# Kernel tuning notes

Hardware: AMD Instinct MI355X
Metric: run time of the kernel (lower is better)

The kernel has to match this reference:

```python
import jax, jax.numpy as jnp
import numpy as np


def gcn_conv(x, src, dst, norm, W, b, n_nodes):
    # PyG GCNConv: out[dst] = sum_edges norm * (x @ W)[src] + b
    h = x @ W                      # [N, F_out]
    msg = h[src] * norm[:, None]   # [E', F_out] gather + scale
    out = jax.ops.segment_sum(msg, dst, num_segments=n_nodes)
    return out + b


def _gcn_norm(edge_index, n_nodes):
    # add self loops, compute symmetric normalization deg^-1/2[src]*deg^-1/2[dst]
    loop = jnp.arange(n_nodes, dtype=edge_index.dtype)
    src = jnp.concatenate([edge_index[0], loop])
    dst = jnp.concatenate([edge_index[1], loop])
    deg = jnp.zeros((n_nodes,), jnp.float32).at[dst].add(1.0)
    dinv = jnp.where(deg > 0, jax.lax.rsqrt(deg), 0.0)
    norm = dinv[src] * dinv[dst]
    return src, dst, norm


def setup_inputs() -> dict:
    key = jax.random.key(0)
    ks = jax.random.split(key, 5)
    N, E, C_in, C_out = 50000, 800000, 128, 32
    H = 2 * C_out
    x = jax.random.normal(ks[0], (N, C_in), jnp.float32)
    edge_index = jax.random.randint(ks[1], (2, E), 0, N, jnp.int64)
    s1 = 1.0 / np.sqrt(C_in)
    s2 = 1.0 / np.sqrt(H)
    W1 = jax.random.uniform(ks[2], (C_in, H), jnp.float32, -s1, s1)
    b1 = jnp.zeros((H,), jnp.float32)
    W_mu = jax.random.uniform(ks[3], (H, C_out), jnp.float32, -s2, s2)
    b_mu = jnp.zeros((C_out,), jnp.float32)
    W_ls = jax.random.uniform(ks[4], (H, C_out), jnp.float32, -s2, s2)
    b_ls = jnp.zeros((C_out,), jnp.float32)
    return {"x": x, "edge_index": edge_index, "W1": W1, "b1": b1,
            "W_mu": W_mu, "b_mu": b_mu, "W_ls": W_ls, "b_ls": b_ls}


def reference(x, edge_index, W1, b1, W_mu, b_mu, W_ls, b_ls):
    n_nodes = x.shape[0]
    src, dst, norm = _gcn_norm(edge_index, n_nodes)
    h = jax.nn.relu(gcn_conv(x, src, dst, norm, W1, b1, n_nodes))
    mu = gcn_conv(h, src, dst, norm, W_mu, b_mu, n_nodes)
    logstd = gcn_conv(h, src, dst, norm, W_ls, b_ls, n_nodes)
    return mu, logstd
```

## Files before the change

kernel.cpp:

```cpp
#include <hip/hip_runtime.h>
#include <hip/hip_fp16.h>
#include <math.h>


typedef unsigned int uint;
typedef unsigned short ushort;
typedef __attribute__((ext_vector_type(8))) short short8;
typedef __attribute__((ext_vector_type(4))) float f32x4;

__device__ __forceinline__ ushort f2bf(float x) {
    uint u = __float_as_uint(x);
    u += 0x7fffu + ((u >> 16) & 1u);
    return (ushort)(u >> 16);
}
__device__ __forceinline__ float bf2f(ushort h) {
    return __uint_as_float((uint)h << 16);
}

__global__ __launch_bounds__(256) void k_hist(
        const int* __restrict__ dst, int* __restrict__ bcount, int E) {
    __shared__ int h[256];
    const int tid = threadIdx.x;
    h[tid] = 0;
    __syncthreads();
    const int base = blockIdx.x * 2048;
    #pragma unroll
    for (int k = 0; k < 8; ++k) {
        int i = base + k * 256 + tid;
        if (i < E) {
            int d = __builtin_nontemporal_load(dst + i);
            atomicAdd(&h[d >> 8], 1);
        }
    }
    __syncthreads();
    if (h[tid]) atomicAdd(&bcount[tid], h[tid]);
}

__global__ __launch_bounds__(256) void k_scatterA(
        const int* __restrict__ src, const int* __restrict__ dst,
        const int* __restrict__ bcount, int* __restrict__ bcursor,
        uint* __restrict__ recs, int E) {
    __shared__ int h[256];
    __shared__ int p[256];
    __shared__ int rb[256];
    const int tid = threadIdx.x;
    h[tid] = 0;
    __syncthreads();
    const int base = blockIdx.x * 2048;
    uint rec[8]; int rk[8];
    #pragma unroll
    for (int k = 0; k < 8; ++k) {
        int i = base + k * 256 + tid;
        if (i < E) {
            int s = __builtin_nontemporal_load(src + i);
            int d = __builtin_nontemporal_load(dst + i);
            int b = d >> 8;
            rec[k] = (uint)s | ((uint)(d & 255) << 16) | ((uint)b << 24);
            rk[k] = atomicAdd(&h[b], 1);
        }
    }
    int v = bcount[tid];
    p[tid] = v;
    __syncthreads();
    #pragma unroll
    for (int off = 1; off < 256; off <<= 1) {
        int x = (tid >= off) ? p[tid - off] : 0;
        __syncthreads();
        p[tid] += x;
        __syncthreads();
    }
    const int excl = p[tid] - v;
    const int hv = h[tid];
    rb[tid] = excl + (hv ? atomicAdd(&bcursor[tid], hv) : 0);
    __syncthreads();
    #pragma unroll
    for (int k = 0; k < 8; ++k) {
        int i = base + k * 256 + tid;
        if (i < E) recs[rb[rec[k] >> 24] + rk[k]] = rec[k];
    }
}

__global__ __launch_bounds__(256, 4) void k_phaseB(
        const uint* __restrict__ recs, const int* __restrict__ bcount,
        int* __restrict__ row_ptr, float* __restrict__ dinv,
        ushort* __restrict__ edges, int N, int E, int NBUCK) {
    __shared__ int h[256];
    __shared__ int p[256];
    __shared__ uint rstage[8192];
    const int tid = threadIdx.x;
    const int bx  = blockIdx.x;
    int v = bcount[tid];
    p[tid] = v;
    h[tid] = 0;
    __syncthreads();
    #pragma unroll
    for (int off = 1; off < 256; off <<= 1) {
        int x = (tid >= off) ? p[tid - off] : 0;
        __syncthreads();
        p[tid] += x;
        __syncthreads();
    }
    const int cnt = bcount[bx];
    const int bs  = p[bx] - cnt;
    const bool stg = (cnt <= 8192);
    for (int i = tid; i < cnt; i += 256) {
        uint r = recs[bs + i];
        if (stg) rstage[i] = r;
        atomicAdd(&h[(r >> 16) & 255], 1);
    }
    __syncthreads();
    v = h[tid];
    p[tid] = v;
    __syncthreads();
    #pragma unroll
    for (int off = 1; off < 256; off <<= 1) {
        int x = (tid >= off) ? p[tid - off] : 0;
        __syncthreads();
        p[tid] += x;
        __syncthreads();
    }
    const int excl = p[tid] - v;
    const int node = bx * 256 + tid;
    if (node < N) {
        row_ptr[node] = bs + excl;
        dinv[node] = rsqrtf((float)(v + 1));
    }
    if (bx == NBUCK - 1 && tid == 0) row_ptr[N] = E;
    h[tid] = excl;
    __syncthreads();
    for (int i = tid; i < cnt; i += 256) {
        uint r = stg ? rstage[i] : recs[bs + i];
        int pos = atomicAdd(&h[(r >> 16) & 255], 1);
        edges[bs + pos] = (ushort)(r & 0xffffu);
    }
}

__global__ __launch_bounds__(256, 4) void k_gemm(
        const float* __restrict__ x, const float* __restrict__ W1,
        const float* __restrict__ dinv, ushort* __restrict__ hp, int N) {
    __shared__ ushort Wt[64][136];
    const int tid = threadIdx.x;
    #pragma unroll
    for (int it = 0; it < 8; ++it) {
        int idx = (it * 256 + tid) * 4;
        int k = idx >> 6, c = idx & 63;
        float4 wv = *(const float4*)(W1 + idx);
        Wt[c + 0][k] = f2bf(wv.x);
        Wt[c + 1][k] = f2bf(wv.y);
        Wt[c + 2][k] = f2bf(wv.z);
        Wt[c + 3][k] = f2bf(wv.w);
    }
    __syncthreads();
    const int w = tid >> 6, l = tid & 63;
    const int m = l & 15, q = l >> 4;
    const int row0 = blockIdx.x * 64 + w * 16;
    const size_t arow = (size_t)min(row0 + m, N - 1);
    f32x4 acc0 = {0.f, 0.f, 0.f, 0.f}, acc1 = acc0, acc2 = acc0, acc3 = acc0;
    #pragma unroll
    for (int kc = 0; kc < 4; ++kc) {
        const int kofs = kc * 32 + q * 8;
        const float4* xr = (const float4*)(x + arow * 128 + kofs);
        float4 xa = xr[0], xb = xr[1];
        short8 a;
        a[0] = (short)f2bf(xa.x); a[1] = (short)f2bf(xa.y);
        a[2] = (short)f2bf(xa.z); a[3] = (short)f2bf(xa.w);
        a[4] = (short)f2bf(xb.x); a[5] = (short)f2bf(xb.y);
        a[6] = (short)f2bf(xb.z); a[7] = (short)f2bf(xb.w);
        short8 b0 = *(const short8*)&Wt[m][kofs];
        short8 b1 = *(const short8*)&Wt[m + 16][kofs];
        short8 b2 = *(const short8*)&Wt[m + 32][kofs];
        short8 b3 = *(const short8*)&Wt[m + 48][kofs];
        acc0 = __builtin_amdgcn_mfma_f32_16x16x32_bf16(a, b0, acc0, 0, 0, 0);
        acc1 = __builtin_amdgcn_mfma_f32_16x16x32_bf16(a, b1, acc1, 0, 0, 0);
        acc2 = __builtin_amdgcn_mfma_f32_16x16x32_bf16(a, b2, acc2, 0, 0, 0);
        acc3 = __builtin_amdgcn_mfma_f32_16x16x32_bf16(a, b3, acc3, 0, 0, 0);
    }
    #pragma unroll
    for (int r = 0; r < 4; ++r) {
        int row = row0 + q * 4 + r;
        if (row >= N) continue;
        float dv = dinv[row];
        ushort* hr = hp + (size_t)row * 64 + m;
        hr[0]  = f2bf(acc0[r] * dv);
        hr[16] = f2bf(acc1[r] * dv);
        hr[32] = f2bf(acc2[r] * dv);
        hr[48] = f2bf(acc3[r] * dv);
    }
}

__device__ __forceinline__ void gather_grp8(
        const uint* __restrict__ hp, const ushort* __restrict__ edges,
        int beg, int end, int E, int sl, float4& a0, float4& a1) {
    for (int base = beg; base < end; base += 8) {
        const int mrec = (int)edges[min(base + sl, E - 1)];
        const int cnt = end - base;
        if (cnt >= 8) {
            #pragma unroll
            for (int i = 0; i < 8; ++i) {
                const int r = __shfl(mrec, i, 8);
                const uint4 v = *(const uint4*)(hp + (size_t)r * 32 + 4 * sl);
                a0.x += __uint_as_float(v.x << 16);
                a0.y += __uint_as_float(v.x & 0xffff0000u);
                a0.z += __uint_as_float(v.y << 16);
                a0.w += __uint_as_float(v.y & 0xffff0000u);
                a1.x += __uint_as_float(v.z << 16);
                a1.y += __uint_as_float(v.z & 0xffff0000u);
                a1.z += __uint_as_float(v.w << 16);
                a1.w += __uint_as_float(v.w & 0xffff0000u);
            }
        } else {
            #pragma unroll
            for (int i = 0; i < 7; ++i) {
                const int r = __shfl(mrec, min(i, cnt - 1), 8);
                uint4 v = *(const uint4*)(hp + (size_t)r * 32 + 4 * sl);
                if (i >= cnt) { v.x = 0u; v.y = 0u; v.z = 0u; v.w = 0u; }
                a0.x += __uint_as_float(v.x << 16);
                a0.y += __uint_as_float(v.x & 0xffff0000u);
                a0.z += __uint_as_float(v.y << 16);
                a0.w += __uint_as_float(v.y & 0xffff0000u);
                a1.x += __uint_as_float(v.z << 16);
                a1.y += __uint_as_float(v.z & 0xffff0000u);
                a1.z += __uint_as_float(v.w << 16);
                a1.w += __uint_as_float(v.w & 0xffff0000u);
            }
        }
    }
}

__global__ __launch_bounds__(256, 6) void k_gather1(
        const uint* __restrict__ hp, const int* __restrict__ row_ptr,
        const ushort* __restrict__ edges, const float* __restrict__ dinv,
        const float* __restrict__ b1, uint* __restrict__ ho, int N, int E) {
    const int lane = threadIdx.x & 63;
    const int sl = lane & 7;
    const int n = blockIdx.x * 32 + ((threadIdx.x >> 6) << 3) + (lane >> 3);
    const int nc = min(n, N - 1);
    const int beg = row_ptr[nc], end = row_ptr[nc + 1];
    float4 a0 = {0.f, 0.f, 0.f, 0.f}, a1 = a0;
    gather_grp8(hp, edges, beg, end, E, sl, a0, a1);
    const float dv = dinv[nc];
    const uint4 sv = *(const uint4*)(hp + (size_t)nc * 32 + 4 * sl);
    const float4 bA = ((const float4*)b1)[2 * sl];
    const float4 bB = ((const float4*)b1)[2 * sl + 1];
    float s0 = a0.x + bf2f((ushort)sv.x);
    float s1 = a0.y + bf2f((ushort)(sv.x >> 16));
    float s2 = a0.z + bf2f((ushort)sv.y);
    float s3 = a0.w + bf2f((ushort)(sv.y >> 16));
    float s4 = a1.x + bf2f((ushort)sv.z);
    float s5 = a1.y + bf2f((ushort)(sv.z >> 16));
    float s6 = a1.z + bf2f((ushort)sv.w);
    float s7 = a1.w + bf2f((ushort)(sv.w >> 16));
    float h0 = fmaxf(fmaf(dv, s0, bA.x), 0.f) * dv;
    float h1 = fmaxf(fmaf(dv, s1, bA.y), 0.f) * dv;
    float h2 = fmaxf(fmaf(dv, s2, bA.z), 0.f) * dv;
    float h3 = fmaxf(fmaf(dv, s3, bA.w), 0.f) * dv;
    float h4 = fmaxf(fmaf(dv, s4, bB.x), 0.f) * dv;
    float h5 = fmaxf(fmaf(dv, s5, bB.y), 0.f) * dv;
    float h6 = fmaxf(fmaf(dv, s6, bB.z), 0.f) * dv;
    float h7 = fmaxf(fmaf(dv, s7, bB.w), 0.f) * dv;
    if (n < N) {
        uint4 o;
        o.x = (uint)f2bf(h0) | ((uint)f2bf(h1) << 16);
        o.y = (uint)f2bf(h2) | ((uint)f2bf(h3) << 16);
        o.z = (uint)f2bf(h4) | ((uint)f2bf(h5) << 16);
        o.w = (uint)f2bf(h6) | ((uint)f2bf(h7) << 16);
        *(uint4*)(ho + (size_t)n * 32 + 4 * sl) = o;
    }
}

__global__ __launch_bounds__(256, 6) void k_gather2(
        const uint* __restrict__ hp, const int* __restrict__ row_ptr,
        const ushort* __restrict__ edges, const float* __restrict__ dinv,
        const float* __restrict__ Wmu, const float* __restrict__ Wls,
        const float* __restrict__ bmu, const float* __restrict__ bls,
        float* __restrict__ out, int N, int E) {
    __shared__ __align__(16) float hs[4][8][64];
    const int lane = threadIdx.x & 63;
    const int sl = lane & 7, grp = lane >> 3;
    const int w = threadIdx.x >> 6;
    const int n = blockIdx.x * 32 + (w << 3) + grp;
    const int nc = min(n, N - 1);
    const int beg = row_ptr[nc], end = row_ptr[nc + 1];
    float4 a0 = {0.f, 0.f, 0.f, 0.f}, a1 = a0;
    gather_grp8(hp, edges, beg, end, E, sl, a0, a1);
    const float dv = dinv[nc];
    const uint4 sv = *(const uint4*)(hp + (size_t)nc * 32 + 4 * sl);
    float4 gA, gB;
    gA.x = dv * (a0.x + bf2f((ushort)sv.x));
    gA.y = dv * (a0.y + bf2f((ushort)(sv.x >> 16)));
    gA.z = dv * (a0.z + bf2f((ushort)sv.y));
    gA.w = dv * (a0.w + bf2f((ushort)(sv.y >> 16)));
    gB.x = dv * (a1.x + bf2f((ushort)sv.z));
    gB.y = dv * (a1.y + bf2f((ushort)(sv.z >> 16)));
    gB.z = dv * (a1.z + bf2f((ushort)sv.w));
    gB.w = dv * (a1.w + bf2f((ushort)(sv.w >> 16)));
    *(float4*)&hs[w][grp][8 * sl]     = gA;
    *(float4*)&hs[w][grp][8 * sl + 4] = gB;
    const float* Wsel = (lane < 32) ? (Wmu + lane) : (Wls + (lane - 32));
    const float bias  = (lane < 32) ? bmu[lane] : bls[lane - 32];
    #pragma unroll
    for (int p = 0; p < 2; ++p) {
        float c0 = 0.f, c1 = 0.f, c2 = 0.f, c3 = 0.f;
        #pragma unroll 4
        for (int k = 0; k < 64; ++k) {
            float wv = Wsel[k * 32];
            c0 = fmaf(hs[w][p * 4 + 0][k], wv, c0);
            c1 = fmaf(hs[w][p * 4 + 1][k], wv, c1);
            c2 = fmaf(hs[w][p * 4 + 2][k], wv, c2);
            c3 = fmaf(hs[w][p * 4 + 3][k], wv, c3);
        }
        const int n0 = blockIdx.x * 32 + (w << 3) + p * 4;
        float cs[4] = {c0, c1, c2, c3};
        #pragma unroll
        for (int gg = 0; gg < 4; ++gg) {
            int nn = n0 + gg;
            if (nn >= N) break;
            float t = cs[gg] + bias;
            if (lane < 32) out[(size_t)nn * 32 + lane] = t;
            else           out[(size_t)N * 32 + (size_t)nn * 32 + (lane - 32)] = t;
        }
    }
}

extern "C" void kernel_launch(void* const* d_in, const int* in_sizes, int n_in,
                              void* d_out, int out_size, void* d_ws, size_t ws_size,
                              hipStream_t stream) {
    const float* x   = (const float*)d_in[0];
    const int*   ei  = (const int*)d_in[1];
    const float* W1  = (const float*)d_in[2];
    const float* b1  = (const float*)d_in[3];
    const float* Wmu = (const float*)d_in[4];
    const float* bmu = (const float*)d_in[5];
    const float* Wls = (const float*)d_in[6];
    const float* bls = (const float*)d_in[7];
    float* out = (float*)d_out;

    const int N = in_sizes[0] / 128;
    const int E = in_sizes[1] / 2;
    const int* src = ei;
    const int* dst = ei + E;
    const int HB    = (E + 2047) / 2048;
    const int NBUCK = (N + 255) / 256;
    const int GB    = (N + 63) / 64;
    const int NG    = (N + 31) / 32;

    char* w = (char*)d_ws;
    auto carve = [&](size_t bytes) { char* p = w; w += (bytes + 1023) & ~(size_t)1023; return p; };
    int*    bcount  = (int*)   carve(512 * 4);
    int*    bcursor = bcount + 256;
    uint*   recs    = (uint*)  carve((size_t)E * 4);
    int*    row_ptr = (int*)   carve((size_t)(N + 1) * 4);
    float*  dinv    = (float*) carve((size_t)N * 4);
    ushort* edges   = (ushort*)carve((size_t)E * 2);
    ushort* h_pre   = (ushort*)carve((size_t)N * 64 * 2);
    ushort* h_mid   = (ushort*)carve((size_t)N * 64 * 2);

    hipMemsetAsync(bcount, 0, 512 * 4, stream);
    k_hist    <<<HB, 256, 0, stream>>>(dst, bcount, E);
    k_scatterA<<<HB, 256, 0, stream>>>(src, dst, bcount, bcursor, recs, E);
    k_phaseB  <<<NBUCK, 256, 0, stream>>>(recs, bcount, row_ptr, dinv, edges, N, E, NBUCK);
    k_gemm    <<<GB, 256, 0, stream>>>(x, W1, dinv, h_pre, N);
    k_gather1 <<<NG, 256, 0, stream>>>((const uint*)h_pre, row_ptr, edges, dinv,
                                       b1, (uint*)h_mid, N, E);
    k_gather2 <<<NG, 256, 0, stream>>>((const uint*)h_mid, row_ptr, edges, dinv,
                                       Wmu, Wls, bmu, bls, out, N, E);
}
```

Measured before the change: 182.1 us.

## Split hidden features into two 32-wide halves and gather each half separately

The GEMM now writes the 64-wide bf16 hidden features as two separate 32-column arrays. Each SpMM gather pass runs once per half, with 4 lanes per node instead of 8. This shrinks the per-pass working set (N×64B per half), so gathered rows are more likely to stay in L2/MALL cache. The second layer stores the first half's aggregation as fp32 and combines it with the second half in a final kernel that uses an XOR-swizzled shared buffer to avoid LDS bank conflicts. In exchange, the edge list and row pointers are read twice per layer, there are extra launches, and an fp32 intermediate is written and read back.

Measured after the change: 201.7 us. 10.7% more time.

```diff
diff --git a/kernel.cpp b/kernel.cpp
--- a/kernel.cpp
+++ b/kernel.cpp
@@ -137,7 +137,8 @@
 
 __global__ __launch_bounds__(256, 4) void k_gemm(
         const float* __restrict__ x, const float* __restrict__ W1,
-        const float* __restrict__ dinv, ushort* __restrict__ hp, int N) {
+        const float* __restrict__ dinv, ushort* __restrict__ hpA,
+        ushort* __restrict__ hpB, int N) {
     __shared__ ushort Wt[64][136];
     const int tid = threadIdx.x;
     #pragma unroll
@@ -180,68 +181,68 @@
         int row = row0 + q * 4 + r;
         if (row >= N) continue;
         float dv = dinv[row];
-        ushort* hr = hp + (size_t)row * 64 + m;
-        hr[0]  = f2bf(acc0[r] * dv);
-        hr[16] = f2bf(acc1[r] * dv);
-        hr[32] = f2bf(acc2[r] * dv);
-        hr[48] = f2bf(acc3[r] * dv);
-    }
-}
-
-__device__ __forceinline__ void gather_grp8(
-        const uint* __restrict__ hp, const ushort* __restrict__ edges,
-        int beg, int end, int E, int sl, float4& a0, float4& a1) {
+        ushort* hrA = hpA + (size_t)row * 32 + m;
+        hrA[0]  = f2bf(acc0[r] * dv);
+        hrA[16] = f2bf(acc1[r] * dv);
+        ushort* hrB = hpB + (size_t)row * 32 + m;
+        hrB[0]  = f2bf(acc2[r] * dv);
+        hrB[16] = f2bf(acc3[r] * dv);
+    }
+}
+
+__device__ __forceinline__ void acc8(const uint4 v, float4& a0, float4& a1) {
+    a0.x += __uint_as_float(v.x << 16);
+    a0.y += __uint_as_float(v.x & 0xffff0000u);
+    a0.z += __uint_as_float(v.y << 16);
+    a0.w += __uint_as_float(v.y & 0xffff0000u);
+    a1.x += __uint_as_float(v.z << 16);
+    a1.y += __uint_as_float(v.z & 0xffff0000u);
+    a1.z += __uint_as_float(v.w << 16);
+    a1.w += __uint_as_float(v.w & 0xffff0000u);
+}
+
+__device__ __forceinline__ void gather_grp4(
+        const uint* __restrict__ rows, const ushort* __restrict__ edges,
+        int beg, int end, int E, int j, float4& a0, float4& a1) {
     for (int base = beg; base < end; base += 8) {
-        const int mrec = (int)edges[min(base + sl, E - 1)];
         const int cnt = end - base;
+        const int m0 = (int)edges[min(base + j, E - 1)];
+        const int m1 = (int)edges[min(base + 4 + j, E - 1)];
         if (cnt >= 8) {
             #pragma unroll
             for (int i = 0; i < 8; ++i) {
-                const int r = __shfl(mrec, i, 8);
-                const uint4 v = *(const uint4*)(hp + (size_t)r * 32 + 4 * sl);
-                a0.x += __uint_as_float(v.x << 16);
-                a0.y += __uint_as_float(v.x & 0xffff0000u);
-                a0.z += __uint_as_float(v.y << 16);
-                a0.w += __uint_as_float(v.y & 0xffff0000u);
-                a1.x += __uint_as_float(v.z << 16);
-                a1.y += __uint_as_float(v.z & 0xffff0000u);
-                a1.z += __uint_as_float(v.w << 16);
-                a1.w += __uint_as_float(v.w & 0xffff0000u);
+                const int r = __shfl(i < 4 ? m0 : m1, i & 3, 4);
+                const uint4 v = *(const uint4*)(rows + (size_t)r * 16 + 4 * j);
+                acc8(v, a0, a1);
             }
         } else {
             #pragma unroll
             for (int i = 0; i < 7; ++i) {
-                const int r = __shfl(mrec, min(i, cnt - 1), 8);
-                uint4 v = *(const uint4*)(hp + (size_t)r * 32 + 4 * sl);
+                const int e = min(i, cnt - 1);
+                const int r = __shfl(e < 4 ? m0 : m1, e & 3, 4);
+                uint4 v = *(const uint4*)(rows + (size_t)r * 16 + 4 * j);
                 if (i >= cnt) { v.x = 0u; v.y = 0u; v.z = 0u; v.w = 0u; }
-                a0.x += __uint_as_float(v.x << 16);
-                a0.y += __uint_as_float(v.x & 0xffff0000u);
-                a0.z += __uint_as_float(v.y << 16);
-                a0.w += __uint_as_float(v.y & 0xffff0000u);
-                a1.x += __uint_as_float(v.z << 16);
-                a1.y += __uint_as_float(v.z & 0xffff0000u);
-                a1.z += __uint_as_float(v.w << 16);
-                a1.w += __uint_as_float(v.w & 0xffff0000u);
+                acc8(v, a0, a1);
             }
         }
     }
 }
 
-__global__ __launch_bounds__(256, 6) void k_gather1(
-        const uint* __restrict__ hp, const int* __restrict__ row_ptr,
+__global__ __launch_bounds__(256, 6) void k_gl1(
+        const uint* __restrict__ hpH, const int* __restrict__ row_ptr,
         const ushort* __restrict__ edges, const float* __restrict__ dinv,
-        const float* __restrict__ b1, uint* __restrict__ ho, int N, int E) {
+        const float* __restrict__ b1H, uint* __restrict__ midH, int N, int E) {
     const int lane = threadIdx.x & 63;
-    const int sl = lane & 7;
-    const int n = blockIdx.x * 32 + ((threadIdx.x >> 6) << 3) + (lane >> 3);
+    const int j = lane & 3, grp = lane >> 2;
+    const int n = blockIdx.x * 64 + ((threadIdx.x >> 6) << 4) + grp;
     const int nc = min(n, N - 1);
     const int beg = row_ptr[nc], end = row_ptr[nc + 1];
     float4 a0 = {0.f, 0.f, 0.f, 0.f}, a1 = a0;
-    gather_grp8(hp, edges, beg, end, E, sl, a0, a1);
+    gather_grp4(hpH, edges, beg, end, E, j, a0, a1);
     const float dv = dinv[nc];
-    const uint4 sv = *(const uint4*)(hp + (size_t)nc * 32 + 4 * sl);
-    const float4 bA = ((const float4*)b1)[2 * sl];
-    const float4 bB = ((const float4*)b1)[2 * sl + 1];
+    const uint4 sv = *(const uint4*)(hpH + (size_t)nc * 16 + 4 * j);
+    const float4 bA = *(const float4*)(b1H + 8 * j);
+    const float4 bB = *(const float4*)(b1H + 8 * j + 4);
     float s0 = a0.x + bf2f((ushort)sv.x);
     float s1 = a0.y + bf2f((ushort)(sv.x >> 16));
     float s2 = a0.z + bf2f((ushort)sv.y);
@@ -264,56 +265,91 @@
         o.y = (uint)f2bf(h2) | ((uint)f2bf(h3) << 16);
         o.z = (uint)f2bf(h4) | ((uint)f2bf(h5) << 16);
         o.w = (uint)f2bf(h6) | ((uint)f2bf(h7) << 16);
-        *(uint4*)(ho + (size_t)n * 32 + 4 * sl) = o;
-    }
-}
-
-__global__ __launch_bounds__(256, 6) void k_gather2(
-        const uint* __restrict__ hp, const int* __restrict__ row_ptr,
+        *(uint4*)(midH + (size_t)n * 16 + 4 * j) = o;
+    }
+}
+
+__global__ __launch_bounds__(256, 6) void k_gl2a(
+        const uint* __restrict__ midH, const int* __restrict__ row_ptr,
         const ushort* __restrict__ edges, const float* __restrict__ dinv,
+        float* __restrict__ gH, int N, int E) {
+    const int lane = threadIdx.x & 63;
+    const int j = lane & 3, grp = lane >> 2;
+    const int n = blockIdx.x * 64 + ((threadIdx.x >> 6) << 4) + grp;
+    const int nc = min(n, N - 1);
+    const int beg = row_ptr[nc], end = row_ptr[nc + 1];
+    float4 a0 = {0.f, 0.f, 0.f, 0.f}, a1 = a0;
+    gather_grp4(midH, edges, beg, end, E, j, a0, a1);
+    const float dv = dinv[nc];
+    const uint4 sv = *(const uint4*)(midH + (size_t)nc * 16 + 4 * j);
+    float4 g0, g1;
+    g0.x = dv * (a0.x + bf2f((ushort)sv.x));
+    g0.y = dv * (a0.y + bf2f((ushort)(sv.x >> 16)));
+    g0.z = dv * (a0.z + bf2f((ushort)sv.y));
+    g0.w = dv * (a0.w + bf2f((ushort)(sv.y >> 16)));
+    g1.x = dv * (a1.x + bf2f((ushort)sv.z));
+    g1.y = dv * (a1.y + bf2f((ushort)(sv.z >> 16)));
+    g1.z = dv * (a1.z + bf2f((ushort)sv.w));
+    g1.w = dv * (a1.w + bf2f((ushort)(sv.w >> 16)));
+    if (n < N) {
+        *(float4*)(gH + (size_t)n * 32 + 8 * j)     = g0;
+        *(float4*)(gH + (size_t)n * 32 + 8 * j + 4) = g1;
+    }
+}
+
+__global__ __launch_bounds__(256, 6) void k_gl2b(
+        const uint* __restrict__ midH, const float* __restrict__ gA,
+        const int* __restrict__ row_ptr, const ushort* __restrict__ edges,
+        const float* __restrict__ dinv,
         const float* __restrict__ Wmu, const float* __restrict__ Wls,
         const float* __restrict__ bmu, const float* __restrict__ bls,
         float* __restrict__ out, int N, int E) {
-    __shared__ __align__(16) float hs[4][8][64];
+    __shared__ float hs[4][1024];
     const int lane = threadIdx.x & 63;
-    const int sl = lane & 7, grp = lane >> 3;
+    const int j = lane & 3, grp = lane >> 2;
     const int w = threadIdx.x >> 6;
-    const int n = blockIdx.x * 32 + (w << 3) + grp;
+    const int n = blockIdx.x * 64 + (w << 4) + grp;
     const int nc = min(n, N - 1);
     const int beg = row_ptr[nc], end = row_ptr[nc + 1];
     float4 a0 = {0.f, 0.f, 0.f, 0.f}, a1 = a0;
-    gather_grp8(hp, edges, beg, end, E, sl, a0, a1);
+    gather_grp4(midH, edges, beg, end, E, j, a0, a1);
     const float dv = dinv[nc];
-    const uint4 sv = *(const uint4*)(hp + (size_t)nc * 32 + 4 * sl);
-    float4 gA, gB;
-    gA.x = dv * (a0.x + bf2f((ushort)sv.x));
-    gA.y = dv * (a0.y + bf2f((ushort)(sv.x >> 16)));
-    gA.z = dv * (a0.z + bf2f((ushort)sv.y));
-    gA.w = dv * (a0.w + bf2f((ushort)(sv.y >> 16)));
-    gB.x = dv * (a1.x + bf2f((ushort)sv.z));
-    gB.y = dv * (a1.y + bf2f((ushort)(sv.z >> 16)));
-    gB.z = dv * (a1.z + bf2f((ushort)sv.w));
-    gB.w = dv * (a1.w + bf2f((ushort)(sv.w >> 16)));
-    *(float4*)&hs[w][grp][8 * sl]     = gA;
-    *(float4*)&hs[w][grp][8 * sl + 4] = gB;
+    const uint4 sv = *(const uint4*)(midH + (size_t)nc * 16 + 4 * j);
+    float4 gb0, gb1;
+    gb0.x = dv * (a0.x + bf2f((ushort)sv.x));
+    gb0.y = dv * (a0.y + bf2f((ushort)(sv.x >> 16)));
+    gb0.z = dv * (a0.z + bf2f((ushort)sv.y));
+    gb0.w = dv * (a0.w + bf2f((ushort)(sv.y >> 16)));
+    gb1.x = dv * (a1.x + bf2f((ushort)sv.z));
+    gb1.y = dv * (a1.y + bf2f((ushort)(sv.z >> 16)));
+    gb1.z = dv * (a1.z + bf2f((ushort)sv.w));
+    gb1.w = dv * (a1.w + bf2f((ushort)(sv.w >> 16)));
+    const float4 ga0 = *(const float4*)(gA + (size_t)nc * 32 + 8 * j);
+    const float4 ga1 = *(const float4*)(gA + (size_t)nc * 32 + 8 * j + 4);
+    *(float4*)&hs[w][grp * 64 + ((2 * j)     ^ grp) * 4] = ga0;
+    *(float4*)&hs[w][grp * 64 + ((2 * j + 1) ^ grp) * 4] = ga1;
+    *(float4*)&hs[w][grp * 64 + ((8 + 2 * j) ^ grp) * 4] = gb0;
+    *(float4*)&hs[w][grp * 64 + ((9 + 2 * j) ^ grp) * 4] = gb1;
     const float* Wsel = (lane < 32) ? (Wmu + lane) : (Wls + (lane - 32));
     const float bias  = (lane < 32) ? bmu[lane] : bls[lane - 32];
-    #pragma unroll
-    for (int p = 0; p < 2; ++p) {
+    const int n0 = blockIdx.x * 64 + (w << 4);
+    #pragma unroll
+    for (int p = 0; p < 4; ++p) {
+        const int r0 = p * 4;
         float c0 = 0.f, c1 = 0.f, c2 = 0.f, c3 = 0.f;
         #pragma unroll 4
         for (int k = 0; k < 64; ++k) {
-            float wv = Wsel[k * 32];
-            c0 = fmaf(hs[w][p * 4 + 0][k], wv, c0);
-            c1 = fmaf(hs[w][p * 4 + 1][k], wv, c1);
-            c2 = fmaf(hs[w][p * 4 + 2][k], wv, c2);
-            c3 = fmaf(hs[w][p * 4 + 3][k], wv, c3);
+            const float wv = Wsel[k * 32];
+            const int kc = k >> 2, kk = k & 3;
+            c0 = fmaf(hs[w][(r0 + 0) * 64 + ((kc ^ (r0 + 0)) * 4) + kk], wv, c0);
+            c1 = fmaf(hs[w][(r0 + 1) * 64 + ((kc ^ (r0 + 1)) * 4) + kk], wv, c1);
+            c2 = fmaf(hs[w][(r0 + 2) * 64 + ((kc ^ (r0 + 2)) * 4) + kk], wv, c2);
+            c3 = fmaf(hs[w][(r0 + 3) * 64 + ((kc ^ (r0 + 3)) * 4) + kk], wv, c3);
         }
-        const int n0 = blockIdx.x * 32 + (w << 3) + p * 4;
         float cs[4] = {c0, c1, c2, c3};
         #pragma unroll
         for (int gg = 0; gg < 4; ++gg) {
-            int nn = n0 + gg;
+            int nn = n0 + r0 + gg;
             if (nn >= N) break;
             float t = cs[gg] + bias;
             if (lane < 32) out[(size_t)nn * 32 + lane] = t;
@@ -342,7 +378,7 @@
     const int HB    = (E + 2047) / 2048;
     const int NBUCK = (N + 255) / 256;
     const int GB    = (N + 63) / 64;
-    const int NG    = (N + 31) / 32;
+    const int NG    = (N + 63) / 64;
 
     char* w = (char*)d_ws;
     auto carve = [&](size_t bytes) { char* p = w; w += (bytes + 1023) & ~(size_t)1023; return p; };
@@ -352,16 +388,23 @@
     int*    row_ptr = (int*)   carve((size_t)(N + 1) * 4);
     float*  dinv    = (float*) carve((size_t)N * 4);
     ushort* edges   = (ushort*)carve((size_t)E * 2);
-    ushort* h_pre   = (ushort*)carve((size_t)N * 64 * 2);
-    ushort* h_mid   = (ushort*)carve((size_t)N * 64 * 2);
+    ushort* hpA     = (ushort*)carve((size_t)N * 32 * 2);
+    ushort* hpB     = (ushort*)carve((size_t)N * 32 * 2);
+    ushort* midA    = (ushort*)carve((size_t)N * 32 * 2);
+    ushort* midB    = (ushort*)carve((size_t)N * 32 * 2);
+    float*  gA      = (float*) carve((size_t)N * 32 * 4);
 
     hipMemsetAsync(bcount, 0, 512 * 4, stream);
     k_hist    <<<HB, 256, 0, stream>>>(dst, bcount, E);
     k_scatterA<<<HB, 256, 0, stream>>>(src, dst, bcount, bcursor, recs, E);
     k_phaseB  <<<NBUCK, 256, 0, stream>>>(recs, bcount, row_ptr, dinv, edges, N, E, NBUCK);
-    k_gemm    <<<GB, 256, 0, stream>>>(x, W1, dinv, h_pre, N);
-    k_gather1 <<<NG, 256, 0, stream>>>((const uint*)h_pre, row_ptr, edges, dinv,
-                                       b1, (uint*)h_mid, N, E);
-    k_gather2 <<<NG, 256, 0, stream>>>((const uint*)h_mid, row_ptr, edges, dinv,
+    k_gemm    <<<GB, 256, 0, stream>>>(x, W1, dinv, hpA, hpB, N);
+    k_gl1     <<<NG, 256, 0, stream>>>((const uint*)hpA, row_ptr, edges, dinv,
+                                       b1, (uint*)midA, N, E);
+    k_gl1     <<<NG, 256, 0, stream>>>((const uint*)hpB, row_ptr, edges, dinv,
+                                       b1 + 32, (uint*)midB, N, E);
+    k_gl2a    <<<NG, 256, 0, stream>>>((const uint*)midA, row_ptr, edges, dinv,
+                                       gA, N, E);
+    k_gl2b    <<<NG, 256, 0, stream>>>((const uint*)midB, gA, row_ptr, edges, dinv,
                                        Wmu, Wls, bmu, bls, out, N, E);
 }
```
